# Kernel optimization log

Hardware: AMD Instinct MI355X
Metric: run time of the kernel (lower is better)

The kernel has to match this reference:

```python
import jax, jax.numpy as jnp
import numpy as np

B = 1024      # graphs (frames)
P = 23        # nodes per frame (22 players + ball)
N = B * P     # total nodes
F = 14        # input node features
D = 256       # hidden dim
H = 4         # attention heads
Dh = D // H   # per-head dim
L = 3         # GATv2 layers
C = 23        # receiver classes
NEG_SLOPE = 0.2


def setup_inputs() -> dict:
    key = jax.random.key(0)
    ks = jax.random.split(key, 20)
    x = jax.random.normal(ks[0], (N, F), jnp.float32)
    # complete directed graph (no self loops) within each frame
    a = np.arange(P)
    s, d = np.meshgrid(a, a, indexing='ij')
    m = s != d
    s, d = s[m], d[m]                      # [P*(P-1)] = 506
    offs = (np.arange(B) * P)[:, None]
    src = (s[None, :] + offs).reshape(-1)
    dst = (d[None, :] + offs).reshape(-1)
    edge_index = jnp.asarray(np.stack([src, dst]), jnp.int32)   # [2, E]
    batch = jnp.asarray(np.repeat(np.arange(B), P), jnp.int32)  # [N]
    g = lambda k, shape, fan: jax.random.normal(k, shape, jnp.float32) / np.sqrt(fan)
    return {
        'x': x, 'edge_index': edge_index, 'batch': batch,
        # input projection F -> D
        'W_in': g(ks[1], (F, D), F), 'b_in': jnp.zeros((D,), jnp.float32),
        # stacked GATv2 layer params (all D -> D)
        'Wl': g(ks[2], (L, D, H, Dh), D), 'Wr': g(ks[3], (L, D, H, Dh), D),
        'att': g(ks[4], (L, H, Dh), Dh),
        # receiver head: D -> D -> C
        'Wr1': g(ks[5], (D, D), D), 'br1': jnp.zeros((D,), jnp.float32),
        'Wr2': g(ks[6], (D, C), D), 'br2': jnp.zeros((C,), jnp.float32),
        # shot head: receiver embedding + concat MLP 2D -> D -> 1
        'E_recv': g(ks[7], (C, D), D),
        'Ws1': g(ks[8], (2 * D, D), 2 * D), 'bs1': jnp.zeros((D,), jnp.float32),
        'Ws2': g(ks[9], (D, 1), D), 'bs2': jnp.zeros((1,), jnp.float32),
    }


def _gatv2_layer(h, src, dst, Wl, Wr, att):
    # GATv2: e_ij = a^T LeakyReLU(Wl h_j + Wr h_i); msg = alpha_ij * Wl h_j
    hl = jnp.einsum('nd,dhk->nhk', h, Wl)               # [N,H,Dh]
    hr = jnp.einsum('nd,dhk->nhk', h, Wr)
    e = jax.nn.leaky_relu(hl[src] + hr[dst], NEG_SLOPE) # [E,H,Dh]
    scores = jnp.einsum('ehk,hk->eh', e, att)           # [E,H]
    # segment softmax over incoming edges of each dst node
    smax = jax.ops.segment_max(scores, dst, num_segments=N)   # [N,H]
    ex = jnp.exp(scores - smax[dst])
    denom = jax.ops.segment_sum(ex, dst, num_segments=N)      # [N,H]
    alpha = ex / denom[dst]                                    # [E,H]
    msg = hl[src] * alpha[..., None]                           # [E,H,Dh]
    out = jax.ops.segment_sum(msg, dst, num_segments=N).reshape(N, H * Dh)
    return jax.nn.elu(out + h)  # residual + activation


def reference(x, edge_index, batch, W_in, b_in, Wl, Wr, att,
              Wr1, br1, Wr2, br2, E_recv, Ws1, bs1, Ws2, bs2):
    src, dst = edge_index[0], edge_index[1]
    h = x @ W_in + b_in                                   # [N,D]
    for l in range(L):
        h = _gatv2_layer(h, src, dst, Wl[l], Wr[l], att[l])
    # mean readout per graph
    cnt = jax.ops.segment_sum(jnp.ones((N,), h.dtype), batch, num_segments=B)
    g = jax.ops.segment_sum(h, batch, num_segments=B) / cnt[:, None]  # [B,D]
    # receiver distribution
    recv_logits = jax.nn.relu(g @ Wr1 + br1) @ Wr2 + br2  # [B,C]
    recv_probs = jax.nn.softmax(recv_logits, axis=1)
    # shot logit for every (graph, receiver) pair, fully batched
    z = jnp.concatenate([
        jnp.broadcast_to(g[:, None, :], (B, C, D)),
        jnp.broadcast_to(E_recv[None, :, :], (B, C, D)),
    ], axis=-1)                                           # [B,C,2D]
    shot_bc = (jax.nn.relu(z @ Ws1 + bs1) @ Ws2 + bs2)[..., 0]  # [B,C]
    # marginalize: expected shot logit under receiver distribution
    return jnp.sum(shot_bc * recv_probs, axis=1)          # [B]
```

## Files before the change

### kernel.cpp

```cpp
#include <hip/hip_runtime.h>

#define BBATCH 1024
#define NPAIR 512
#define PP 23
#define FF 14
#define DD 256
#define CC 23

#define HSTR 258
#define SLSTR 264
#define RG 47472
#define SL_OFF    (RG)
#define SRO_OFF   (RG + 12144)
#define FRAG_OFF  (RG)
#define ALPHA_OFF (RG + 24576)
#define XS_OFF    (ALPHA_OFF)
#define INVZ_OFF  (ALPHA_OFF + 8192)
#define SMEM_SZ   (INVZ_OFF + 384)

#define GV_OFF    (ALPHA_OFF)
#define T1_OFF    (ALPHA_OFF + 2048)
#define GT_OFF    (ALPHA_OFF + 4096)
#define LG_OFF    (ALPHA_OFF + 6144)
#define PRB_OFF   (ALPHA_OFF + 6400)
#define RED_OFF   (ALPHA_OFF + 6656)

#define SWZB(b) ((b) ^ (((b) >> 3) & 7))
#define SWZC(c) (SWZB((c) >> 3) * 8 + ((c) & 7))

typedef _Float16 f16;
typedef __attribute__((ext_vector_type(8))) _Float16 f16x8;
typedef __attribute__((ext_vector_type(4))) _Float16 f16x4;
typedef __attribute__((ext_vector_type(2))) _Float16 f16x2;
typedef __attribute__((ext_vector_type(4))) float f32x4;

__global__ __launch_bounds__(256) void k_prep(const float* __restrict__ Wl,
    const float* __restrict__ Wr, const float* __restrict__ E,
    const float* __restrict__ Ws1, f16* __restrict__ Bf, float* __restrict__ EB)
{
    __shared__ float ws[DD][16];
    int t = threadIdx.x;
    if (blockIdx.x < 96) {
        int bid = blockIdx.x;
        int ll = bid >> 5, ntile = bid & 31;
        int n0 = ntile * 16;
        const float* W = (n0 < 256) ? (Wl + (size_t)ll * 65536) : (Wr + (size_t)ll * 65536);
        int c0 = n0 & 255;
        for (int kk = t >> 4; kk < DD; kk += 16)
            ws[kk][t & 15] = W[(size_t)kk * 256 + c0 + (t & 15)];
        __syncthreads();
        size_t base = (size_t)bid * 4096;
        for (int idx = t; idx < 4096; idx += 256) {
            int ks = idx >> 9;
            int lane = (idx >> 3) & 63;
            int e = idx & 7;
            int col = lane & 15;
            int k = ks * 32 + ((lane >> 4) << 3) + e;
            Bf[base + idx] = (f16)ws[k][col];
        }
    } else {
        int c = blockIdx.x - 96;
        float acc = 0.f;
        for (int k = 0; k < DD; ++k)
            acc = fmaf(E[c * DD + k], Ws1[(DD + k) * DD + t], acc);
        EB[c * DD + t] = acc;
    }
}

__global__ __launch_bounds__(512, 4) void k_fused(
    const float* __restrict__ x, const float* __restrict__ Win,
    const float* __restrict__ bin, const f16* __restrict__ Bf,
    const float* __restrict__ att,
    const float* __restrict__ Wr1, const float* __restrict__ br1,
    const float* __restrict__ Wr2, const float* __restrict__ br2,
    const float* __restrict__ Ws1, const float* __restrict__ bs1,
    const float* __restrict__ Ws2, const float* __restrict__ bs2,
    const float* __restrict__ EB, float* __restrict__ out)
{
    __shared__ __align__(16) char smem[SMEM_SZ];
    float* hstate = (float*)smem;
    f16* sl16   = (f16*)(smem + SL_OFF);
    f16* sro16  = (f16*)(smem + SRO_OFF);
    f16* frag   = (f16*)(smem + FRAG_OFF);
    f16* aF     = (f16*)(smem + ALPHA_OFF);
    float* xs   = (float*)(smem + XS_OFF);
    float* invZ = (float*)(smem + INVZ_OFF);
    float* gv   = (float*)(smem + GV_OFF);
    float* t1s  = (float*)(smem + T1_OFF);
    float* gts  = (float*)(smem + GT_OFF);
    float* lgs  = (float*)(smem + LG_OFF);
    float* prb  = (float*)(smem + PRB_OFF);
    float* red  = (float*)(smem + RED_OFF);

    int t = threadIdx.x;
    int pair = blockIdx.x;

    for (int idx = t; idx < 46 * FF; idx += 512)
        xs[idx] = x[(size_t)pair * 46 * FF + idx];
    __syncthreads();

    {
        int c2 = (t & 127) * 2, rp = t >> 7;
        float2 bb = *(const float2*)&bin[c2];
        for (int r = rp; r < 48; r += 4) {
            float h0 = 0.f, h1 = 0.f;
            if (r < 46) {
                h0 = bb.x; h1 = bb.y;
#pragma unroll
                for (int f = 0; f < FF; ++f) {
                    float xv = xs[r * FF + f];
                    float2 wv = *(const float2*)&Win[f * DD + c2];
                    h0 = fmaf(xv, wv.x, h0);
                    h1 = fmaf(xv, wv.y, h1);
                }
                *(float2*)&hstate[r * HSTR + c2] = make_float2(h0, h1);
            }
            int off = ((r >> 4) * 8 + (c2 >> 5)) * 512 +
                      ((r & 15) + (((c2 & 31) >> 3) << 4)) * 8 + (c2 & 7);
            f16x2 hv2 = { (f16)h0, (f16)h1 };
            *(f16x2*)(frag + off) = hv2;
        }
    }

    int ln = t & 63, w = t >> 6;

    int sc_i  = t >> 4;
    int sc_ch = t & 15;
    int sc_hh = sc_ch >> 2;
    bool sc_act = (t < 368);
    int sb0 = SWZB(2 * sc_ch) * 8;
    int sb1 = SWZB(2 * sc_ch + 1) * 8;

    for (int layer = 0; layer < 3; ++layer) {
        if (layer > 0) {
            int c2 = (t & 127) * 2, rp = t >> 7;
            for (int r = rp; r < 48; r += 4) {
                float h0 = 0.f, h1 = 0.f;
                if (r < 46) {
                    float2 hv = *(const float2*)&hstate[r * HSTR + c2];
                    h0 = hv.x; h1 = hv.y;
                }
                int off = ((r >> 4) * 8 + (c2 >> 5)) * 512 +
                          ((r & 15) + (((c2 & 31) >> 3) << 4)) * 8 + (c2 & 7);
                f16x2 hv2 = { (f16)h0, (f16)h1 };
                *(f16x2*)(frag + off) = hv2;
            }
        }
        __syncthreads();

        if (layer == 0)
            *(f32x4*)(smem + ALPHA_OFF + t * 16) = (f32x4)0.f;

        const f16* pB = Bf + (size_t)layer * 131072 + (size_t)(w * 4) * 4096 + ln * 8;
        const f16* lA = frag + ln * 8;

        f32x4 acc[3][4];
#pragma unroll
        for (int mt = 0; mt < 3; ++mt)
#pragma unroll
            for (int nt = 0; nt < 4; ++nt) acc[mt][nt] = (f32x4)0.0f;

        __builtin_amdgcn_s_setprio(1);
#pragma unroll
        for (int ks = 0; ks < 8; ++ks) {
            f16x8 a0 = *(const f16x8*)(lA + (0 * 8 + ks) * 512);
            f16x8 a1 = *(const f16x8*)(lA + (1 * 8 + ks) * 512);
            f16x8 a2 = *(const f16x8*)(lA + (2 * 8 + ks) * 512);
#pragma unroll
            for (int nt = 0; nt < 4; ++nt) {
                f16x8 b = *(const f16x8*)(pB + (nt * 8 + ks) * 512);
                acc[0][nt] = __builtin_amdgcn_mfma_f32_16x16x32_f16(a0, b, acc[0][nt], 0, 0, 0);
                acc[1][nt] = __builtin_amdgcn_mfma_f32_16x16x32_f16(a1, b, acc[1][nt], 0, 0, 0);
                acc[2][nt] = __builtin_amdgcn_mfma_f32_16x16x32_f16(a2, b, acc[2][nt], 0, 0, 0);
            }
        }
        __builtin_amdgcn_s_setprio(0);
        __syncthreads();

        for (int f = 0; f < 2; ++f) {
#pragma unroll
            for (int mt = 0; mt < 3; ++mt) {
                int rbase = mt * 16 + (ln >> 4) * 4;
#pragma unroll
                for (int nt = 0; nt < 4; ++nt) {
                    int col = w * 64 + nt * 16 + (ln & 15);
                    f16* dst = (col < 256) ? sl16 : sro16;
                    int cc = col & 255;
                    int sc = SWZC(cc);
#pragma unroll
                    for (int r2 = 0; r2 < 4; ++r2) {
                        int i = rbase + r2 - f * PP;
                        if (0 <= i && i < PP) dst[i * SLSTR + sc] = (f16)acc[mt][nt][r2];
                    }
                }
            }
            __syncthreads();

            if (sc_act) {
                const float* ap = att + layer * DD + sc_ch * 16;
                float4 af0 = *(const float4*)(ap);
                float4 af1 = *(const float4*)(ap + 4);
                float4 af2 = *(const float4*)(ap + 8);
                float4 af3 = *(const float4*)(ap + 12);
                f16x8 av0 = { (f16)af0.x, (f16)af0.y, (f16)af0.z, (f16)af0.w,
                              (f16)af1.x, (f16)af1.y, (f16)af1.z, (f16)af1.w };
                f16x8 av1 = { (f16)af2.x, (f16)af2.y, (f16)af2.z, (f16)af2.w,
                              (f16)af3.x, (f16)af3.y, (f16)af3.z, (f16)af3.w };
                const f16* srp = sro16 + sc_i * SLSTR;
                f16x8 rv0 = *(const f16x8*)(srp + sb0);
                f16x8 rv1 = *(const f16x8*)(srp + sb1);
                int wbase = ((sc_hh * 2 + (sc_i >> 4)) << 9) + ((sc_i & 15) << 3);
#pragma unroll 2
                for (int j = 0; j < PP; ++j) {
                    const f16* slp = sl16 + j * SLSTR;
                    f16x8 v0 = *(const f16x8*)(slp + sb0) + rv0;
                    f16x8 v1 = *(const f16x8*)(slp + sb1) + rv1;
                    v0 = __builtin_elementwise_max(v0, v0 * (f16)0.2f);
                    v1 = __builtin_elementwise_max(v1, v1 * (f16)0.2f);
                    f16x8 tot = av0 * v0;
                    tot += av1 * v1;
                    f16x4 t4 = __builtin_shufflevector(tot, tot, 0, 1, 2, 3) +
                               __builtin_shufflevector(tot, tot, 4, 5, 6, 7);
                    float p = (float)t4[0] + (float)t4[1] + (float)t4[2] + (float)t4[3];
                    p += __shfl_xor(p, 1, 64);
                    p += __shfl_xor(p, 2, 64);
                    if ((t & 3) == 0)
                        aF[wbase + ((j >> 3) << 7) + (j & 7)] =
                            (j == sc_i) ? (f16)(-60000.0f) : (f16)p;
                }
            }
            __syncthreads();

            if (t < 368) {
                int i = t >> 4, hh = (t >> 2) & 3, q = t & 3;
                int base = ((hh * 2 + (i >> 4)) << 9) + ((i & 15) << 3);
                float m = -1e30f;
                for (int j = q; j < PP; j += 4)
                    m = fmaxf(m, (float)aF[base + ((j >> 3) << 7) + (j & 7)]);
                m = fmaxf(m, __shfl_xor(m, 1, 64));
                m = fmaxf(m, __shfl_xor(m, 2, 64));
                float s = 0.f;
                for (int j = q; j < PP; j += 4) {
                    f16* p = aF + base + ((j >> 3) << 7) + (j & 7);
                    f16 e = (f16)__expf((float)*p - m);
                    *p = e;
                    s += (float)e;
                }
                s += __shfl_xor(s, 1, 64);
                s += __shfl_xor(s, 2, 64);
                if (q == 0) invZ[i * 4 + hh] = 1.f / s;
            }
            __syncthreads();

            {
                int h = w >> 1, mt = w & 1;
                f16x8 afrag = *(const f16x8*)(aF + ((h * 2 + mt) << 9) + ln * 8);
                int k0 = (ln >> 4) * 8;
                int cb = h * 64 + (ln & 15);
                __builtin_amdgcn_s_setprio(1);
#pragma unroll
                for (int nt = 0; nt < 4; ++nt) {
                    int c = cb + nt * 16;
                    int scn = SWZC(c);
                    f16x8 bfrag;
#pragma unroll
                    for (int e = 0; e < 8; ++e)
                        bfrag[e] = sl16[(k0 + e) * SLSTR + scn];
                    f32x4 a4 = __builtin_amdgcn_mfma_f32_16x16x32_f16(
                        afrag, bfrag, (f32x4)0.0f, 0, 0, 0);
#pragma unroll
                    for (int r2 = 0; r2 < 4; ++r2) {
                        int i = mt * 16 + (ln >> 4) * 4 + r2;
                        if (i < PP) {
                            int r = f * PP + i;
                            float res = a4[r2] * invZ[i * 4 + h] + hstate[r * HSTR + c];
                            hstate[r * HSTR + c] = (res > 0.f) ? res : (__expf(res) - 1.f);
                        }
                    }
                }
                __builtin_amdgcn_s_setprio(0);
            }
            __syncthreads();
        }
    }

    {
        int f = t >> 8, c = t & 255;
        float s = 0.f;
#pragma unroll
        for (int i = 0; i < PP; ++i) s += hstate[(f * PP + i) * HSTR + c];
        gv[f * 256 + c] = s * (1.0f / 23.0f);
    }
    __syncthreads();

    {
        int gg = t >> 8, c = t & 255;
        const float* gp = gv + gg * 256;
        float a1 = 0.f, a2 = 0.f;
        for (int k = 0; k < DD; k += 2) {
            float g0 = gp[k], g1 = gp[k + 1];
            a1 = fmaf(g0, Wr1[k * DD + c], a1);
            a1 = fmaf(g1, Wr1[(k + 1) * DD + c], a1);
            a2 = fmaf(g0, Ws1[k * DD + c], a2);
            a2 = fmaf(g1, Ws1[(k + 1) * DD + c], a2);
        }
        t1s[gg * 256 + c] = fmaxf(a1 + br1[c], 0.f);
        gts[gg * 256 + c] = a2 + bs1[c];
    }
    __syncthreads();

    if (t < 2 * CC) {
        int gg = t / CC, c = t - gg * CC;
        float acc = br2[c];
        const float* tp = t1s + gg * 256;
        for (int d = 0; d < DD; ++d) acc = fmaf(tp[d], Wr2[d * CC + c], acc);
        lgs[gg * CC + c] = acc;
    }
    __syncthreads();

    if (t < 2 * CC) {
        int gg = t / CC, c = t - gg * CC;
        const float* lp = lgs + gg * CC;
        float m = -1e30f;
        for (int cc = 0; cc < CC; ++cc) m = fmaxf(m, lp[cc]);
        float s = 0.f;
        for (int cc = 0; cc < CC; ++cc) s += __expf(lp[cc] - m);
        prb[gg * CC + c] = __expf(lp[c] - m) / s;
    }
    __syncthreads();

    {
        int gg = t >> 8, c = t & 255;
        float gt = gts[gg * 256 + c];
        const float* pp = prb + gg * CC;
        float acc = 0.f;
#pragma unroll
        for (int cls = 0; cls < CC; ++cls)
            acc = fmaf(pp[cls], fmaxf(gt + EB[cls * DD + c], 0.f), acc);
        acc *= Ws2[c];
#pragma unroll
        for (int off = 32; off > 0; off >>= 1) acc += __shfl_down(acc, off, 64);
        if (ln == 0) red[w] = acc;
    }
    __syncthreads();
    if (t < 2)
        out[pair * 2 + t] = red[t * 4] + red[t * 4 + 1] + red[t * 4 + 2] +
                            red[t * 4 + 3] + bs2[0];
}

extern "C" void kernel_launch(void* const* d_in, const int* in_sizes, int n_in,
                              void* d_out, int out_size, void* d_ws, size_t ws_size,
                              hipStream_t stream)
{
    const float* x     = (const float*)d_in[0];
    const float* Win   = (const float*)d_in[3];
    const float* bin   = (const float*)d_in[4];
    const float* Wl    = (const float*)d_in[5];
    const float* Wr    = (const float*)d_in[6];
    const float* att   = (const float*)d_in[7];
    const float* Wr1   = (const float*)d_in[8];
    const float* br1   = (const float*)d_in[9];
    const float* Wr2   = (const float*)d_in[10];
    const float* br2   = (const float*)d_in[11];
    const float* Erecv = (const float*)d_in[12];
    const float* Ws1   = (const float*)d_in[13];
    const float* bs1   = (const float*)d_in[14];
    const float* Ws2   = (const float*)d_in[15];
    const float* bs2   = (const float*)d_in[16];
    float* out = (float*)d_out;

    f16* Bf   = (f16*)d_ws;
    float* EB = (float*)(Bf + (size_t)3 * 131072);

    k_prep<<<dim3(96 + CC), dim3(256), 0, stream>>>(Wl, Wr, Erecv, Ws1, Bf, EB);
    k_fused<<<dim3(NPAIR), dim3(512), 0, stream>>>(x, Win, bin, Bf, att,
        Wr1, br1, Wr2, br2, Ws1, bs1, Ws2, bs2, EB, out);
}
```

Measured before the change: 145.7 us.

## Keep GAT hidden state only in fp16 MFMA fragment layout, drop fp32 copy

Removes the fp32 hidden-state buffer in shared memory. The residual, ELU and mean readout now read and write the fp16 fragment-layout buffer directly. This also drops the per-layer repacking loop that converted fp32 state into fp16 fragments. Shared memory per block shrinks enough that more blocks may fit per CU, at the cost of accumulating the residual stream in fp16, which risks accuracy drift across layers.

```diff
diff --git a/kernel.cpp b/kernel.cpp
--- a/kernel.cpp
+++ b/kernel.cpp
@@ -7,13 +7,11 @@
 #define DD 256
 #define CC 23
 
-#define HSTR 258
 #define SLSTR 264
-#define RG 47472
-#define SL_OFF    (RG)
-#define SRO_OFF   (RG + 12144)
-#define FRAG_OFF  (RG)
-#define ALPHA_OFF (RG + 24576)
+#define FRAG_OFF  0
+#define SL_OFF    24576
+#define SRO_OFF   (SL_OFF + 12144)
+#define ALPHA_OFF (SRO_OFF + 12144)
 #define XS_OFF    (ALPHA_OFF)
 #define INVZ_OFF  (ALPHA_OFF + 8192)
 #define SMEM_SZ   (INVZ_OFF + 384)
@@ -33,6 +31,11 @@
 typedef __attribute__((ext_vector_type(4))) _Float16 f16x4;
 typedef __attribute__((ext_vector_type(2))) _Float16 f16x2;
 typedef __attribute__((ext_vector_type(4))) float f32x4;
+
+__device__ __forceinline__ int frag_off(int r, int c) {
+    return ((r >> 4) * 8 + (c >> 5)) * 512 +
+           ((r & 15) + (((c & 31) >> 3) << 4)) * 8 + (c & 7);
+}
 
 __global__ __launch_bounds__(256) void k_prep(const float* __restrict__ Wl,
     const float* __restrict__ Wr, const float* __restrict__ E,
@@ -78,10 +81,9 @@
     const float* __restrict__ EB, float* __restrict__ out)
 {
     __shared__ __align__(16) char smem[SMEM_SZ];
-    float* hstate = (float*)smem;
+    f16* frag   = (f16*)(smem + FRAG_OFF);
     f16* sl16   = (f16*)(smem + SL_OFF);
     f16* sro16  = (f16*)(smem + SRO_OFF);
-    f16* frag   = (f16*)(smem + FRAG_OFF);
     f16* aF     = (f16*)(smem + ALPHA_OFF);
     float* xs   = (float*)(smem + XS_OFF);
     float* invZ = (float*)(smem + INVZ_OFF);
@@ -113,12 +115,9 @@
                     h0 = fmaf(xv, wv.x, h0);
                     h1 = fmaf(xv, wv.y, h1);
                 }
-                *(float2*)&hstate[r * HSTR + c2] = make_float2(h0, h1);
-            }
-            int off = ((r >> 4) * 8 + (c2 >> 5)) * 512 +
-                      ((r & 15) + (((c2 & 31) >> 3) << 4)) * 8 + (c2 & 7);
+            }
             f16x2 hv2 = { (f16)h0, (f16)h1 };
-            *(f16x2*)(frag + off) = hv2;
+            *(f16x2*)(frag + frag_off(r, c2)) = hv2;
         }
     }
 
@@ -132,20 +131,6 @@
     int sb1 = SWZB(2 * sc_ch + 1) * 8;
 
     for (int layer = 0; layer < 3; ++layer) {
-        if (layer > 0) {
-            int c2 = (t & 127) * 2, rp = t >> 7;
-            for (int r = rp; r < 48; r += 4) {
-                float h0 = 0.f, h1 = 0.f;
-                if (r < 46) {
-                    float2 hv = *(const float2*)&hstate[r * HSTR + c2];
-                    h0 = hv.x; h1 = hv.y;
-                }
-                int off = ((r >> 4) * 8 + (c2 >> 5)) * 512 +
-                          ((r & 15) + (((c2 & 31) >> 3) << 4)) * 8 + (c2 & 7);
-                f16x2 hv2 = { (f16)h0, (f16)h1 };
-                *(f16x2*)(frag + off) = hv2;
-            }
-        }
         __syncthreads();
 
         if (layer == 0)
@@ -272,9 +257,9 @@
                     for (int r2 = 0; r2 < 4; ++r2) {
                         int i = mt * 16 + (ln >> 4) * 4 + r2;
                         if (i < PP) {
-                            int r = f * PP + i;
-                            float res = a4[r2] * invZ[i * 4 + h] + hstate[r * HSTR + c];
-                            hstate[r * HSTR + c] = (res > 0.f) ? res : (__expf(res) - 1.f);
+                            int fo = frag_off(f * PP + i, c);
+                            float res = a4[r2] * invZ[i * 4 + h] + (float)frag[fo];
+                            frag[fo] = (f16)((res > 0.f) ? res : (__expf(res) - 1.f));
                         }
                     }
                 }
@@ -288,7 +273,7 @@
         int f = t >> 8, c = t & 255;
         float s = 0.f;
 #pragma unroll
-        for (int i = 0; i < PP; ++i) s += hstate[(f * PP + i) * HSTR + c];
+        for (int i = 0; i < PP; ++i) s += (float)frag[frag_off(f * PP + i, c)];
         gv[f * 256 + c] = s * (1.0f / 23.0f);
     }
     __syncthreads();
```

Result: no change. 146.9 us (+0.8%).
